# Optimization experiments

Measured on AMD Instinct MI355X. Metric: run time of the kernel, lower is better.

Reference implementation:

```python
import jax, jax.numpy as jnp
import numpy as np

N_EMBD = 1024
HEAD_SIZE = 64
N_HEADS = 16
BLOCK_SIZE = 2048


def setup_inputs() -> dict:
    key = jax.random.key(0)
    ks = jax.random.split(key, 7)
    s = 0.02
    return {
        "X": jax.random.normal(ks[0], (2, BLOCK_SIZE, N_EMBD), dtype=jnp.float32),
        # per-head projection weights, torch Linear layout [out, in] stacked over heads
        "Wq": jax.random.normal(ks[1], (N_HEADS, HEAD_SIZE, N_EMBD), dtype=jnp.float32) * s,
        "Wk": jax.random.normal(ks[2], (N_HEADS, HEAD_SIZE, N_EMBD), dtype=jnp.float32) * s,
        "Wv": jax.random.normal(ks[3], (N_HEADS, HEAD_SIZE, N_EMBD), dtype=jnp.float32) * s,
        "Wp": jax.random.normal(ks[4], (N_EMBD, N_EMBD), dtype=jnp.float32) * s,
        "bp": jax.random.normal(ks[5], (N_EMBD,), dtype=jnp.float32) * s,
    }


def reference(X, Wq, Wk, Wv, Wp, bp):
    B, T, C = X.shape
    # per-head projections: [B,H,T,D]
    q = jnp.einsum("btc,hdc->bhtd", X, Wq)
    k = jnp.einsum("btc,hdc->bhtd", X, Wk)
    v = jnp.einsum("btc,hdc->bhtd", X, Wv)
    # NOTE: original scales by C**-0.5 where C = n_embd (not head_size)
    scores = jnp.einsum("bhtd,bhsd->bhts", q, k) * (C ** -0.5)  # [B,H,T,T]
    causal = jnp.tril(jnp.ones((T, T), dtype=bool))
    scores = jnp.where(causal, scores, -jnp.inf)
    weights = jax.nn.softmax(scores, axis=-1)
    out = jnp.einsum("bhts,bhsd->bhtd", weights, v)  # [B,H,T,D]
    # concat heads along last dim: [B,T,H*D]
    out = out.transpose(0, 2, 1, 3).reshape(B, T, -1)
    # output projection (dropout is identity in eval)
    return out @ Wp.T + bp
```

## Files before the change

kernel.cpp:

```cpp
#include <hip/hip_runtime.h>
#include <hip/hip_bf16.h>

typedef __bf16 bf16_t;
typedef __bf16 bf16x8 __attribute__((ext_vector_type(8)));
typedef __bf16 bf16x4 __attribute__((ext_vector_type(4)));
typedef float  f32x4  __attribute__((ext_vector_type(4)));

#define MFMA16(a,b,c) __builtin_amdgcn_mfma_f32_16x16x32_bf16(a,b,c,0,0,0)

constexpr int B_ = 2, T_ = 2048, H_ = 16, D_ = 64, C_ = 1024;
constexpr int GK = C_;

typedef const __attribute__((address_space(1))) unsigned char ga_t;
typedef __attribute__((address_space(3))) unsigned char la_t;
__device__ __forceinline__ void gld16(const void* g, void* l) {
  __builtin_amdgcn_global_load_lds((ga_t*)g, (la_t*)l, 16, 0, 0);
}

__global__ __launch_bounds__(256) void cast_all(
    const float* __restrict__ X,  const float* __restrict__ Wq,
    const float* __restrict__ Wk, const float* __restrict__ Wv,
    const float* __restrict__ Wp,
    bf16_t* __restrict__ Xb,  bf16_t* __restrict__ Wqb, bf16_t* __restrict__ Wkb,
    bf16_t* __restrict__ Wvb, bf16_t* __restrict__ Wpb)
{
  int i = blockIdx.x * 256 + threadIdx.x;
  const float* src; bf16_t* dst; int off;
  if      (i < 1048576) { src = X;  dst = Xb;  off = i; }
  else if (i < 1310720) { src = Wq; dst = Wqb; off = i - 1048576; }
  else if (i < 1572864) { src = Wk; dst = Wkb; off = i - 1310720; }
  else if (i < 1835008) { src = Wv; dst = Wvb; off = i - 1572864; }
  else                  { src = Wp; dst = Wpb; off = i - 1835008; }
  float4 v = *reinterpret_cast<const float4*>(src + (size_t)off * 4);
  bf16x4 o;
  o[0] = (bf16_t)v.x; o[1] = (bf16_t)v.y; o[2] = (bf16_t)v.z; o[3] = (bf16_t)v.w;
  *reinterpret_cast<bf16x4*>(dst + (size_t)off * 4) = o;
}

__global__ __launch_bounds__(512, 2) void gemm_qkv256(
    const bf16_t* __restrict__ Xb, const bf16_t* __restrict__ Wqkv,
    bf16_t* __restrict__ qo, bf16_t* __restrict__ ko, bf16_t* __restrict__ vto)
{
  __shared__ bf16_t sA[2][256 * 64];
  __shared__ bf16_t sB[2][192 * 64];
  const int tid = threadIdx.x, lane = tid & 63, wid = tid >> 6;
  const int wm = wid >> 1, wn = wid & 1;
  const int g = lane >> 4, c = lane & 15, rk = c & 7;
  const int bx = blockIdx.x, by = blockIdx.y;
  const int srow = tid >> 3;
  const int sg   = (tid & 7) ^ (srow & 7);
  const bf16_t* asrc = Xb   + (size_t)(bx * 256 + srow) * GK + sg * 8;
  const bf16_t* bsrc = Wqkv + (size_t)(by * 192 + srow) * GK + sg * 8;
  f32x4 acc[4][6] = {};

  #define STG(buf, kt)                                                        \
    { char* da = (char*)sA + (buf) * 32768;                                   \
      char* db = (char*)sB + (buf) * 24576;                                   \
      _Pragma("unroll")                                                       \
      for (int it = 0; it < 4; ++it)                                          \
        gld16(asrc + (size_t)it * 65536 + (kt) * 64, da + (it * 512 + tid) * 16); \
      _Pragma("unroll")                                                       \
      for (int it = 0; it < 3; ++it)                                          \
        gld16(bsrc + (size_t)it * 65536 + (kt) * 64, db + (it * 512 + tid) * 16); \
    }

  #define ITER(t, buf)                                                        \
    {                                                                         \
      if ((t) < 15) asm volatile("s_waitcnt vmcnt(7)");                       \
      else          asm volatile("s_waitcnt vmcnt(0)");                       \
      __builtin_amdgcn_s_barrier();             \
      __builtin_amdgcn_sched_barrier(0);                                      \
      const char* ca = (const char*)sA + (buf) * 32768;                       \
      const char* cb = (const char*)sB + (buf) * 24576;                       \
      bf16x8 af[4][2], bfr[6][2];                                             \
      _Pragma("unroll")                                                       \
      for (int mi = 0; mi < 4; ++mi)                                          \
        _Pragma("unroll")                                                     \
        for (int ks = 0; ks < 2; ++ks)                                        \
          af[mi][ks] = *reinterpret_cast<const bf16x8*>(                      \
              ca + (wm * 64 + mi * 16 + c) * 128 + (((ks * 4 + g) ^ rk) * 16)); \
      _Pragma("unroll")                                                       \
      for (int ni = 0; ni < 6; ++ni)                                          \
        _Pragma("unroll")                                                     \
        for (int ks = 0; ks < 2; ++ks)                                        \
          bfr[ni][ks] = *reinterpret_cast<const bf16x8*>(                     \
              cb + (wn * 96 + ni * 16 + c) * 128 + (((ks * 4 + g) ^ rk) * 16)); \
      asm volatile("s_waitcnt lgkmcnt(0)");         \
      __builtin_amdgcn_sched_barrier(0);                                      \
      __builtin_amdgcn_s_barrier();                \
      __builtin_amdgcn_sched_barrier(0);                                      \
      if ((t) + 2 < 16) STG(buf, (t) + 2);           \
      __builtin_amdgcn_s_setprio(1);                                          \
      _Pragma("unroll")                                                       \
      for (int ks = 0; ks < 2; ++ks)                                          \
        _Pragma("unroll")                                                     \
        for (int mi = 0; mi < 4; ++mi)                                        \
          _Pragma("unroll")                                                   \
          for (int ni = 0; ni < 6; ++ni)                                      \
            acc[mi][ni] = MFMA16(af[mi][ks], bfr[ni][ks], acc[mi][ni]);       \
      __builtin_amdgcn_s_setprio(0);                                          \
    }

  STG(0, 0);
  STG(1, 1);
  #pragma unroll 1
  for (int t0 = 0; t0 < 16; t0 += 2) {
    ITER(t0, 0);
    ITER(t0 + 1, 1);
  }
  #undef ITER
  #undef STG

  const float qscale = 0.04508422002778f;
  #pragma unroll
  for (int ni = 0; ni < 6; ++ni) {
    int col  = by * 192 + wn * 96 + ni * 16 + c;
    int mode = col >> 10;
    int cm   = col & 1023;
    int h = cm >> 6, d = cm & 63;
    #pragma unroll
    for (int mi = 0; mi < 4; ++mi) {
      int row0 = bx * 256 + wm * 64 + mi * 16 + g * 4;
      int b = row0 >> 11, tt0 = row0 & 2047;
      if (mode == 2) {
        bf16x4 wv;
        #pragma unroll
        for (int r = 0; r < 4; ++r) wv[r] = (bf16_t)acc[mi][ni][r];
        *reinterpret_cast<bf16x4*>(
            &vto[((size_t)(b * H_ + h) * D_ + d) * T_ + tt0]) = wv;
      } else {
        bf16_t* dst = (mode == 0) ? qo : ko;
        float   sc  = (mode == 0) ? qscale : 1.0f;
        #pragma unroll
        for (int r = 0; r < 4; ++r)
          dst[((size_t)(b * H_ + h) * T_ + (tt0 + r)) * D_ + d] =
              (bf16_t)(acc[mi][ni][r] * sc);
      }
    }
  }
}

__global__ __launch_bounds__(128, 2) void attn_fwd(
    const bf16_t* __restrict__ q, const bf16_t* __restrict__ k,
    const bf16_t* __restrict__ vt, bf16_t* __restrict__ att)
{
  __shared__ bf16_t sK[2][64 * 64], sV[2][64 * 64];
  __shared__ bf16_t sP[2][2][16 * 64];
  const int tid = threadIdx.x, lane = tid & 63, w = tid >> 6;
  const int g = lane >> 4, c = lane & 15;
  const int bid = blockIdx.x;
  const int qt = 31 - (bid >> 5);
  const int bh = bid & 31;
  const bf16_t* qb = q  + (size_t)bh * T_ * D_;
  const bf16_t* kb = k  + (size_t)bh * T_ * D_;
  const bf16_t* vb = vt + (size_t)bh * D_ * T_;

  bf16x8 qa[2][2];
  #pragma unroll
  for (int gg = 0; gg < 2; ++gg)
    #pragma unroll
    for (int ks = 0; ks < 2; ++ks)
      qa[gg][ks] = *reinterpret_cast<const bf16x8*>(
          qb + (size_t)(qt * 64 + w * 32 + gg * 16 + c) * D_ + ks * 32 + g * 8);

  const int srow = tid >> 3, sgr0 = tid & 7;
  #define STAGE(buf, kt)                                                        \
    {                                                                           \
      char* kdst = (char*)sK + (size_t)(buf) * 8192;                            \
      char* vdst = (char*)sV + (size_t)(buf) * 8192;                            \
      _Pragma("unroll")                                                         \
      for (int it = 0; it < 4; ++it) {                                          \
        int idx = it * 128 + tid;                                               \
        int row = it * 16 + srow;                                               \
        int sg  = sgr0 ^ (row & 7);                                             \
        gld16(kb + (size_t)((kt) * 64 + row) * D_ + sg * 8, kdst + idx * 16);   \
        gld16(vb + (size_t)row * T_ + (kt) * 64 + sg * 8,   vdst + idx * 16);   \
      }                                                                         \
    }

  STAGE(0, 0);

  float m_r[2] = {-3.0e38f, -3.0e38f}, l_r[2] = {0.f, 0.f};
  f32x4 acc_t[2][4] = {};
  const int rowK = c & 7;

  for (int kt = 0; kt <= qt; ++kt) {
    const int cur = kt & 1;
    __syncthreads();
    if (kt < qt) STAGE(cur ^ 1, kt + 1);

    const char* kc = (char*)sK + (size_t)cur * 8192;
    const char* vc = (char*)sV + (size_t)cur * 8192;
    bf16x8 kf[2][4], vf[2][4];
    #pragma unroll
    for (int ks = 0; ks < 2; ++ks)
      #pragma unroll
      for (int f = 0; f < 4; ++f) {
        int rb = (f * 16 + c) * 128;
        int gsw = ((ks * 4 + g) ^ rowK) * 16;
        kf[ks][f] = *reinterpret_cast<const bf16x8*>(kc + rb + gsw);
        vf[ks][f] = *reinterpret_cast<const bf16x8*>(vc + rb + gsw);
      }

    f32x4 s[2][4] = {};
    __builtin_amdgcn_s_setprio(1);
    #pragma unroll
    for (int gg = 0; gg < 2; ++gg)
      #pragma unroll
      for (int fj = 0; fj < 4; ++fj)
        #pragma unroll
        for (int ks = 0; ks < 2; ++ks)
          s[gg][fj] = MFMA16(kf[ks][fj], qa[gg][ks], s[gg][fj]);
    __builtin_amdgcn_s_setprio(0);

    if (kt == qt) {
      #pragma unroll
      for (int gg = 0; gg < 2; ++gg)
        #pragma unroll
        for (int fj = 0; fj < 4; ++fj)
          #pragma unroll
          for (int r = 0; r < 4; ++r)
            if (fj * 16 + g * 4 + r > w * 32 + gg * 16 + c) s[gg][fj][r] = -1e30f;
    }

    #pragma unroll
    for (int gg = 0; gg < 2; ++gg) {
      float m01 = fmaxf(fmaxf(s[gg][0][0], s[gg][0][1]), fmaxf(s[gg][0][2], s[gg][0][3]));
      float m23 = fmaxf(fmaxf(s[gg][1][0], s[gg][1][1]), fmaxf(s[gg][1][2], s[gg][1][3]));
      float m45 = fmaxf(fmaxf(s[gg][2][0], s[gg][2][1]), fmaxf(s[gg][2][2], s[gg][2][3]));
      float m67 = fmaxf(fmaxf(s[gg][3][0], s[gg][3][1]), fmaxf(s[gg][3][2], s[gg][3][3]));
      float mx = fmaxf(fmaxf(m01, m23), fmaxf(m45, m67));
      mx = fmaxf(mx, __shfl_xor(mx, 16));
      mx = fmaxf(mx, __shfl_xor(mx, 32));

      if (__any(mx > m_r[gg] + 8.f)) {
        float mnew = fmaxf(m_r[gg], mx);
        float sc = __builtin_amdgcn_exp2f(m_r[gg] - mnew);
        l_r[gg] *= sc;
        #pragma unroll
        for (int fd = 0; fd < 4; ++fd)
          #pragma unroll
          for (int r = 0; r < 4; ++r) acc_t[gg][fd][r] *= sc;
        m_r[gg] = mnew;
      }

      char* pc = (char*)sP + (size_t)(w * 2 + gg) * 2048;
      #pragma unroll
      for (int fj = 0; fj < 4; ++fj) {
        bf16x4 pw;
        #pragma unroll
        for (int r = 0; r < 4; ++r) {
          float pe = __builtin_amdgcn_exp2f(s[gg][fj][r] - m_r[gg]);
          l_r[gg] += pe;
          pw[r] = (bf16_t)pe;
        }
        *reinterpret_cast<bf16x4*>(
            pc + c * 128 + (((fj * 2 + (g >> 1)) ^ rowK) * 16) + (g & 1) * 8) = pw;
      }
    }

    #pragma unroll
    for (int gg = 0; gg < 2; ++gg) {
      const char* pc = (const char*)sP + (size_t)(w * 2 + gg) * 2048;
      bf16x8 pf[2];
      #pragma unroll
      for (int ks = 0; ks < 2; ++ks)
        pf[ks] = *reinterpret_cast<const bf16x8*>(
            pc + c * 128 + (((ks * 4 + g) ^ rowK) * 16));
      __builtin_amdgcn_s_setprio(1);
      #pragma unroll
      for (int fd = 0; fd < 4; ++fd)
        #pragma unroll
        for (int ks = 0; ks < 2; ++ks)
          acc_t[gg][fd] = MFMA16(vf[ks][fd], pf[ks], acc_t[gg][fd]);
      __builtin_amdgcn_s_setprio(0);
    }
  }

  const int b = bh >> 4, h = bh & 15;
  #pragma unroll
  for (int gg = 0; gg < 2; ++gg) {
    float lr = l_r[gg];
    lr += __shfl_xor(lr, 16);
    lr += __shfl_xor(lr, 32);
    float inv = 1.0f / lr;
    const int t = qt * 64 + w * 32 + gg * 16 + c;
    #pragma unroll
    for (int fd = 0; fd < 4; ++fd) {
      bf16x4 wv;
      #pragma unroll
      for (int r = 0; r < 4; ++r) wv[r] = (bf16_t)(acc_t[gg][fd][r] * inv);
      int d = fd * 16 + g * 4;
      *reinterpret_cast<bf16x4*>(&att[((size_t)(b * T_ + t) * H_ + h) * D_ + d]) = wv;
    }
  }
  #undef STAGE
}

__global__ __launch_bounds__(512, 2) void gemm_proj(
    const bf16_t* __restrict__ attb, const bf16_t* __restrict__ Wpb,
    const float* __restrict__ bp, float* __restrict__ out)
{
  __shared__ bf16_t sA[2][128 * 64];
  __shared__ bf16_t sB[2][128 * 64];
  const int tid = threadIdx.x, lane = tid & 63, wid = tid >> 6;
  const int wm = wid >> 2, wn = wid & 3;
  const int g = lane >> 4, c = lane & 15, rk = c & 7;
  const int bx = blockIdx.x, by = blockIdx.y;
  const int srow = tid >> 3;
  const int sg   = (tid & 7) ^ (srow & 7);
  const bf16_t* asrc = attb + (size_t)(bx * 128 + srow) * GK + sg * 8;
  const bf16_t* bsrc = Wpb  + (size_t)(by * 128 + srow) * GK + sg * 8;
  f32x4 acc[4][2] = {};

  #define STGP(buf, kt)                                                       \
    { char* da = (char*)sA + (buf) * 16384;                                   \
      char* db = (char*)sB + (buf) * 16384;                                   \
      _Pragma("unroll")                                                       \
      for (int it = 0; it < 2; ++it) {                                        \
        gld16(asrc + (size_t)it * 65536 + (kt) * 64, da + (it * 512 + tid) * 16); \
        gld16(bsrc + (size_t)it * 65536 + (kt) * 64, db + (it * 512 + tid) * 16); \
      } }

  #define ITERP(t, buf)                                                       \
    {                                                                         \
      if ((t) < 15) asm volatile("s_waitcnt vmcnt(4)");                       \
      else          asm volatile("s_waitcnt vmcnt(0)");                       \
      __builtin_amdgcn_s_barrier();                                           \
      __builtin_amdgcn_sched_barrier(0);                                      \
      const char* ca = (const char*)sA + (buf) * 16384;                       \
      const char* cb = (const char*)sB + (buf) * 16384;                       \
      bf16x8 af[4][2], bfr[2][2];                                             \
      _Pragma("unroll")                                                       \
      for (int mi = 0; mi < 4; ++mi)                                          \
        _Pragma("unroll")                                                     \
        for (int ks = 0; ks < 2; ++ks)                                        \
          af[mi][ks] = *reinterpret_cast<const bf16x8*>(                      \
              ca + (wm * 64 + mi * 16 + c) * 128 + (((ks * 4 + g) ^ rk) * 16)); \
      _Pragma("unroll")                                                       \
      for (int ni = 0; ni < 2; ++ni)                                          \
        _Pragma("unroll")                                                     \
        for (int ks = 0; ks < 2; ++ks)                                        \
          bfr[ni][ks] = *reinterpret_cast<const bf16x8*>(                     \
              cb + (wn * 32 + ni * 16 + c) * 128 + (((ks * 4 + g) ^ rk) * 16)); \
      asm volatile("s_waitcnt lgkmcnt(0)");                                   \
      __builtin_amdgcn_sched_barrier(0);                                      \
      __builtin_amdgcn_s_barrier();                                           \
      __builtin_amdgcn_sched_barrier(0);                                      \
      if ((t) + 2 < 16) STGP(buf, (t) + 2);                                   \
      __builtin_amdgcn_s_setprio(1);                                          \
      _Pragma("unroll")                                                       \
      for (int ks = 0; ks < 2; ++ks)                                          \
        _Pragma("unroll")                                                     \
        for (int mi = 0; mi < 4; ++mi)                                        \
          _Pragma("unroll")                                                   \
          for (int ni = 0; ni < 2; ++ni)                                      \
            acc[mi][ni] = MFMA16(af[mi][ks], bfr[ni][ks], acc[mi][ni]);       \
      __builtin_amdgcn_s_setprio(0);                                          \
    }

  STGP(0, 0);
  STGP(1, 1);
  #pragma unroll 1
  for (int t0 = 0; t0 < 16; t0 += 2) {
    ITERP(t0, 0);
    ITERP(t0 + 1, 1);
  }
  #undef ITERP
  #undef STGP

  #pragma unroll
  for (int m = 0; m < 4; ++m)
    #pragma unroll
    for (int n = 0; n < 2; ++n)
      #pragma unroll
      for (int r = 0; r < 4; ++r) {
        int row = bx * 128 + wm * 64 + m * 16 + g * 4 + r;
        int col = by * 128 + wn * 32 + n * 16 + c;
        out[(size_t)row * C_ + col] = acc[m][n][r] + bp[col];
      }
}

extern "C" void kernel_launch(void* const* d_in, const int* in_sizes, int n_in,
                              void* d_out, int out_size, void* d_ws, size_t ws_size,
                              hipStream_t stream)
{
  const float* X  = (const float*)d_in[0];
  const float* Wq = (const float*)d_in[1];
  const float* Wk = (const float*)d_in[2];
  const float* Wv = (const float*)d_in[3];
  const float* Wp = (const float*)d_in[4];
  const float* bp = (const float*)d_in[5];
  float* out = (float*)d_out;

  char* ws = (char*)d_ws;
  bf16_t* Xb   = (bf16_t*)(ws);
  bf16_t* Wqb  = (bf16_t*)(ws + ((size_t)8  << 20));
  bf16_t* Wkb  = (bf16_t*)(ws + ((size_t)10 << 20));
  bf16_t* Wvb  = (bf16_t*)(ws + ((size_t)12 << 20));
  bf16_t* Wpb  = (bf16_t*)(ws + ((size_t)14 << 20));
  bf16_t* qo   = (bf16_t*)(ws + ((size_t)16 << 20));
  bf16_t* ko   = (bf16_t*)(ws + ((size_t)24 << 20));
  bf16_t* vto  = (bf16_t*)(ws + ((size_t)32 << 20));
  bf16_t* attb = (bf16_t*)(ws + ((size_t)40 << 20));

  cast_all<<<8192, 256, 0, stream>>>(X, Wq, Wk, Wv, Wp, Xb, Wqb, Wkb, Wvb, Wpb);
  gemm_qkv256<<<dim3(16, 16), 512, 0, stream>>>(Xb, Wqb, qo, ko, vto);
  attn_fwd<<<1024, 128, 0, stream>>>(qo, ko, vto, attb);
  gemm_proj<<<dim3(32, 8), 512, 0, stream>>>(attb, Wpb, bp, out);
}
```

Measured before the change: 107.0 us.

## Use four waves per attention block with two-deep K/V prefetch pipeline

The attention kernel now runs 256 threads (4 waves, 16 query rows each) instead of 2 waves of 32 rows. Each block still covers the same 64-row query tile, so more waves share each staged K/V tile. K/V staging becomes a three-stage scheme: two tiles are prefetched ahead, with explicit vmcnt waits and split barriers replacing __syncthreads, so loads overlap compute. The aim is more latency hiding and occupancy; the cost is that each wave reloads K/V fragments from LDS for fewer query rows, plus tricky manual waitcnt correctness.

After: 96.16 us. 10.1% less time.

```diff
diff --git a/kernel.cpp b/kernel.cpp
--- a/kernel.cpp
+++ b/kernel.cpp
@@ -140,12 +140,12 @@
   }
 }
 
-__global__ __launch_bounds__(128, 2) void attn_fwd(
+__global__ __launch_bounds__(256, 4) void attn_fwd(
     const bf16_t* __restrict__ q, const bf16_t* __restrict__ k,
     const bf16_t* __restrict__ vt, bf16_t* __restrict__ att)
 {
   __shared__ bf16_t sK[2][64 * 64], sV[2][64 * 64];
-  __shared__ bf16_t sP[2][2][16 * 64];
+  __shared__ bf16_t sP[4][16 * 64];
   const int tid = threadIdx.x, lane = tid & 63, w = tid >> 6;
   const int g = lane >> 4, c = lane & 15;
   const int bid = blockIdx.x;
@@ -155,13 +155,11 @@
   const bf16_t* kb = k  + (size_t)bh * T_ * D_;
   const bf16_t* vb = vt + (size_t)bh * D_ * T_;
 
-  bf16x8 qa[2][2];
+  bf16x8 qa[2];
   #pragma unroll
-  for (int gg = 0; gg < 2; ++gg)
-    #pragma unroll
-    for (int ks = 0; ks < 2; ++ks)
-      qa[gg][ks] = *reinterpret_cast<const bf16x8*>(
-          qb + (size_t)(qt * 64 + w * 32 + gg * 16 + c) * D_ + ks * 32 + g * 8);
+  for (int ks = 0; ks < 2; ++ks)
+    qa[ks] = *reinterpret_cast<const bf16x8*>(
+        qb + (size_t)(qt * 64 + w * 16 + c) * D_ + ks * 32 + g * 8);
 
   const int srow = tid >> 3, sgr0 = tid & 7;
   #define STAGE(buf, kt)                                                        \
@@ -169,9 +167,9 @@
       char* kdst = (char*)sK + (size_t)(buf) * 8192;                            \
       char* vdst = (char*)sV + (size_t)(buf) * 8192;                            \
       _Pragma("unroll")                                                         \
-      for (int it = 0; it < 4; ++it) {                                          \
-        int idx = it * 128 + tid;                                               \
-        int row = it * 16 + srow;                                               \
+      for (int it = 0; it < 2; ++it) {                                          \
+        int idx = it * 256 + tid;                                               \
+        int row = it * 32 + srow;                                               \
         int sg  = sgr0 ^ (row & 7);                                             \
         gld16(kb + (size_t)((kt) * 64 + row) * D_ + sg * 8, kdst + idx * 16);   \
         gld16(vb + (size_t)row * T_ + (kt) * 64 + sg * 8,   vdst + idx * 16);   \
@@ -179,15 +177,19 @@
     }
 
   STAGE(0, 0);
-
-  float m_r[2] = {-3.0e38f, -3.0e38f}, l_r[2] = {0.f, 0.f};
-  f32x4 acc_t[2][4] = {};
+  if (qt >= 1) STAGE(1, 1);
+
+  float m_r = -3.0e38f, l_r = 0.f;
+  f32x4 acc_t[4] = {};
   const int rowK = c & 7;
 
+  #pragma unroll 1
   for (int kt = 0; kt <= qt; ++kt) {
     const int cur = kt & 1;
-    __syncthreads();
-    if (kt < qt) STAGE(cur ^ 1, kt + 1);
+    if (kt < qt) asm volatile("s_waitcnt vmcnt(4)");
+    else         asm volatile("s_waitcnt vmcnt(0)");
+    __builtin_amdgcn_s_barrier();
+    __builtin_amdgcn_sched_barrier(0);
 
     const char* kc = (char*)sK + (size_t)cur * 8192;
     const char* vc = (char*)sV + (size_t)cur * 8192;
@@ -201,98 +203,92 @@
         kf[ks][f] = *reinterpret_cast<const bf16x8*>(kc + rb + gsw);
         vf[ks][f] = *reinterpret_cast<const bf16x8*>(vc + rb + gsw);
       }
-
-    f32x4 s[2][4] = {};
+    asm volatile("s_waitcnt lgkmcnt(0)");
+    __builtin_amdgcn_sched_barrier(0);
+    __builtin_amdgcn_s_barrier();
+    __builtin_amdgcn_sched_barrier(0);
+    if (kt + 2 <= qt) STAGE(cur, kt + 2);
+
+    f32x4 s[4] = {};
     __builtin_amdgcn_s_setprio(1);
     #pragma unroll
-    for (int gg = 0; gg < 2; ++gg)
+    for (int fj = 0; fj < 4; ++fj)
+      #pragma unroll
+      for (int ks = 0; ks < 2; ++ks)
+        s[fj] = MFMA16(kf[ks][fj], qa[ks], s[fj]);
+    __builtin_amdgcn_s_setprio(0);
+
+    if (kt == qt) {
       #pragma unroll
       for (int fj = 0; fj < 4; ++fj)
         #pragma unroll
-        for (int ks = 0; ks < 2; ++ks)
-          s[gg][fj] = MFMA16(kf[ks][fj], qa[gg][ks], s[gg][fj]);
-    __builtin_amdgcn_s_setprio(0);
-
-    if (kt == qt) {
-      #pragma unroll
-      for (int gg = 0; gg < 2; ++gg)
-        #pragma unroll
-        for (int fj = 0; fj < 4; ++fj)
-          #pragma unroll
-          for (int r = 0; r < 4; ++r)
-            if (fj * 16 + g * 4 + r > w * 32 + gg * 16 + c) s[gg][fj][r] = -1e30f;
-    }
-
-    #pragma unroll
-    for (int gg = 0; gg < 2; ++gg) {
-      float m01 = fmaxf(fmaxf(s[gg][0][0], s[gg][0][1]), fmaxf(s[gg][0][2], s[gg][0][3]));
-      float m23 = fmaxf(fmaxf(s[gg][1][0], s[gg][1][1]), fmaxf(s[gg][1][2], s[gg][1][3]));
-      float m45 = fmaxf(fmaxf(s[gg][2][0], s[gg][2][1]), fmaxf(s[gg][2][2], s[gg][2][3]));
-      float m67 = fmaxf(fmaxf(s[gg][3][0], s[gg][3][1]), fmaxf(s[gg][3][2], s[gg][3][3]));
-      float mx = fmaxf(fmaxf(m01, m23), fmaxf(m45, m67));
-      mx = fmaxf(mx, __shfl_xor(mx, 16));
-      mx = fmaxf(mx, __shfl_xor(mx, 32));
-
-      if (__any(mx > m_r[gg] + 8.f)) {
-        float mnew = fmaxf(m_r[gg], mx);
-        float sc = __builtin_amdgcn_exp2f(m_r[gg] - mnew);
-        l_r[gg] *= sc;
-        #pragma unroll
-        for (int fd = 0; fd < 4; ++fd)
-          #pragma unroll
-          for (int r = 0; r < 4; ++r) acc_t[gg][fd][r] *= sc;
-        m_r[gg] = mnew;
-      }
-
-      char* pc = (char*)sP + (size_t)(w * 2 + gg) * 2048;
-      #pragma unroll
-      for (int fj = 0; fj < 4; ++fj) {
-        bf16x4 pw;
-        #pragma unroll
-        for (int r = 0; r < 4; ++r) {
-          float pe = __builtin_amdgcn_exp2f(s[gg][fj][r] - m_r[gg]);
-          l_r[gg] += pe;
-          pw[r] = (bf16_t)pe;
-        }
-        *reinterpret_cast<bf16x4*>(
-            pc + c * 128 + (((fj * 2 + (g >> 1)) ^ rowK) * 16) + (g & 1) * 8) = pw;
-      }
-    }
-
-    #pragma unroll
-    for (int gg = 0; gg < 2; ++gg) {
-      const char* pc = (const char*)sP + (size_t)(w * 2 + gg) * 2048;
-      bf16x8 pf[2];
-      #pragma unroll
-      for (int ks = 0; ks < 2; ++ks)
-        pf[ks] = *reinterpret_cast<const bf16x8*>(
-            pc + c * 128 + (((ks * 4 + g) ^ rowK) * 16));
-      __builtin_amdgcn_s_setprio(1);
+        for (int r = 0; r < 4; ++r)
+          if (fj * 16 + g * 4 + r > w * 16 + c) s[fj][r] = -1e30f;
+    }
+
+    float m01 = fmaxf(fmaxf(s[0][0], s[0][1]), fmaxf(s[0][2], s[0][3]));
+    float m23 = fmaxf(fmaxf(s[1][0], s[1][1]), fmaxf(s[1][2], s[1][3]));
+    float m45 = fmaxf(fmaxf(s[2][0], s[2][1]), fmaxf(s[2][2], s[2][3]));
+    float m67 = fmaxf(fmaxf(s[3][0], s[3][1]), fmaxf(s[3][2], s[3][3]));
+    float mx = fmaxf(fmaxf(m01, m23), fmaxf(m45, m67));
+    mx = fmaxf(mx, __shfl_xor(mx, 16));
+    mx = fmaxf(mx, __shfl_xor(mx, 32));
+
+    if (__any(mx > m_r + 8.f)) {
+      float mnew = fmaxf(m_r, mx);
+      float sc = __builtin_amdgcn_exp2f(m_r - mnew);
+      l_r *= sc;
       #pragma unroll
       for (int fd = 0; fd < 4; ++fd)
         #pragma unroll
-        for (int ks = 0; ks < 2; ++ks)
-          acc_t[gg][fd] = MFMA16(vf[ks][fd], pf[ks], acc_t[gg][fd]);
-      __builtin_amdgcn_s_setprio(0);
-    }
+        for (int r = 0; r < 4; ++r) acc_t[fd][r] *= sc;
+      m_r = mnew;
+    }
+
+    char* pc = (char*)sP + (size_t)w * 2048;
+    float ls[4];
+    #pragma unroll
+    for (int fj = 0; fj < 4; ++fj) {
+      bf16x4 pw;
+      float pe0 = __builtin_amdgcn_exp2f(s[fj][0] - m_r);
+      float pe1 = __builtin_amdgcn_exp2f(s[fj][1] - m_r);
+      float pe2 = __builtin_amdgcn_exp2f(s[fj][2] - m_r);
+      float pe3 = __builtin_amdgcn_exp2f(s[fj][3] - m_r);
+      pw[0] = (bf16_t)pe0; pw[1] = (bf16_t)pe1;
+      pw[2] = (bf16_t)pe2; pw[3] = (bf16_t)pe3;
+      ls[fj] = (pe0 + pe1) + (pe2 + pe3);
+      *reinterpret_cast<bf16x4*>(
+          pc + c * 128 + (((fj * 2 + (g >> 1)) ^ rowK) * 16) + (g & 1) * 8) = pw;
+    }
+    l_r += (ls[0] + ls[1]) + (ls[2] + ls[3]);
+
+    bf16x8 pf[2];
+    #pragma unroll
+    for (int ks = 0; ks < 2; ++ks)
+      pf[ks] = *reinterpret_cast<const bf16x8*>(
+          pc + c * 128 + (((ks * 4 + g) ^ rowK) * 16));
+
+    __builtin_amdgcn_s_setprio(1);
+    #pragma unroll
+    for (int fd = 0; fd < 4; ++fd)
+      #pragma unroll
+      for (int ks = 0; ks < 2; ++ks)
+        acc_t[fd] = MFMA16(vf[ks][fd], pf[ks], acc_t[fd]);
+    __builtin_amdgcn_s_setprio(0);
   }
 
+  l_r += __shfl_xor(l_r, 16);
+  l_r += __shfl_xor(l_r, 32);
+  float inv = 1.0f / l_r;
   const int b = bh >> 4, h = bh & 15;
+  const int t = qt * 64 + w * 16 + c;
   #pragma unroll
-  for (int gg = 0; gg < 2; ++gg) {
-    float lr = l_r[gg];
-    lr += __shfl_xor(lr, 16);
-    lr += __shfl_xor(lr, 32);
-    float inv = 1.0f / lr;
-    const int t = qt * 64 + w * 32 + gg * 16 + c;
-    #pragma unroll
-    for (int fd = 0; fd < 4; ++fd) {
-      bf16x4 wv;
-      #pragma unroll
-      for (int r = 0; r < 4; ++r) wv[r] = (bf16_t)(acc_t[gg][fd][r] * inv);
-      int d = fd * 16 + g * 4;
-      *reinterpret_cast<bf16x4*>(&att[((size_t)(b * T_ + t) * H_ + h) * D_ + d]) = wv;
-    }
+  for (int fd = 0; fd < 4; ++fd) {
+    bf16x4 wv;
+    #pragma unroll
+    for (int r = 0; r < 4; ++r) wv[r] = (bf16_t)(acc_t[fd][r] * inv);
+    int d = fd * 16 + g * 4;
+    *reinterpret_cast<bf16x4*>(&att[((size_t)(b * T_ + t) * H_ + h) * D_ + d]) = wv;
   }
   #undef STAGE
 }
@@ -406,6 +402,6 @@
 
   cast_all<<<8192, 256, 0, stream>>>(X, Wq, Wk, Wv, Wp, Xb, Wqb, Wkb, Wvb, Wpb);
   gemm_qkv256<<<dim3(16, 16), 512, 0, stream>>>(Xb, Wqb, qo, ko, vto);
-  attn_fwd<<<1024, 128, 0, stream>>>(qo, ko, vto, attb);
+  attn_fwd<<<1024, 256, 0, stream>>>(qo, ko, vto, attb);
   gemm_proj<<<dim3(32, 8), 512, 0, stream>>>(attb, Wpb, bp, out);
 }
```
